# Optimization experiments

Measured on AMD Instinct MI355X. Metric: run time of the kernel, lower is better.

The kernel has to match this reference:

```python
import jax, jax.numpy as jnp
import numpy as np

# ---- config constants (from configs) ----
B, L, C = 32, 512, 16
DM, DS, DCONV, EXP, EL = 128, 16, 4, 2, 2
PATCH, STRIDE, PAD, PRED = 16, 8, 8, 96
DIN = EXP * DM            # 256
DTR = (DM + 15) // 16     # dt_rank = 8
NPATCH = (L + 2 * PAD - PATCH) // STRIDE + 1   # 65
HNF = DM * NPATCH         # 8320
EPS = 1e-5


def setup_inputs() -> dict:
    key = jax.random.key(0)
    ks = jax.random.split(key, 14)
    n = jax.random.normal
    A_log = jnp.tile(jnp.log(jnp.arange(1, DS + 1, dtype=jnp.float32)), (EL, DIN, 1))
    return {
        "x_enc": n(ks[0], (B, L, C), jnp.float32),
        "x_mark_enc": n(ks[1], (B, L, 4), jnp.float32),
        "pe_w": n(ks[2], (DM, 1, PATCH), jnp.float32) * (1.0 / np.sqrt(PATCH)),
        "pe_b": n(ks[3], (DM,), jnp.float32) * 0.02,
        "in_proj_w": n(ks[4], (EL, 2 * DIN, DM), jnp.float32) * (1.0 / np.sqrt(DM)),
        "conv_w": n(ks[5], (EL, DIN, DCONV), jnp.float32) * (1.0 / np.sqrt(DCONV)),
        "conv_b": n(ks[6], (EL, DIN), jnp.float32) * 0.02,
        "x_proj_w": n(ks[7], (EL, DTR + 2 * DS, DIN), jnp.float32) * (1.0 / np.sqrt(DIN)),
        "dt_proj_w": n(ks[8], (EL, DIN, DTR), jnp.float32) * (1.0 / np.sqrt(DTR)),
        "dt_proj_b": n(ks[9], (EL, DIN), jnp.float32) * 0.1,
        "A_log": A_log,
        "D": jnp.ones((EL, DIN), jnp.float32),
        "out_proj_w": n(ks[10], (EL, DM, DIN), jnp.float32) * (1.0 / np.sqrt(DIN)),
        "head_w": n(ks[11], (PRED, HNF), jnp.float32) * (1.0 / np.sqrt(HNF)),
    }


def _silu(x):
    return x * jax.nn.sigmoid(x)


def _mamba(x, in_w, cw, cb, xp_w, dtp_w, dtp_b, A_log, Dp, out_w):
    # x: (b, P, DM)
    b = x.shape[0]
    xz = jnp.einsum('bpd,ed->bpe', x, in_w)            # (b, P, 2*DIN)
    xin, z = jnp.split(xz, 2, axis=-1)
    # causal depthwise conv1d over time
    xt = xin.transpose(0, 2, 1)                        # (b, DIN, P)
    conv = jax.lax.conv_general_dilated(
        xt, cw[:, None, :], (1,), [(DCONV - 1, 0)],
        dimension_numbers=('NCH', 'OIH', 'NCH'), feature_group_count=DIN)
    xc = _silu((conv + cb[None, :, None]).transpose(0, 2, 1))   # (b, P, DIN)
    dbc = jnp.einsum('bpd,ed->bpe', xc, xp_w)          # (b, P, DTR+2*DS)
    dt, Bm, Cm = jnp.split(dbc, [DTR, DTR + DS], axis=-1)
    dt = jax.nn.softplus(jnp.einsum('bpr,dr->bpd', dt, dtp_w) + dtp_b)  # (b,P,DIN)
    A = -jnp.exp(A_log)                                # (DIN, DS)

    def step(h, inp):
        dt_t, B_t, C_t, x_t = inp                      # (b,DIN),(b,DS),(b,DS),(b,DIN)
        dA = jnp.exp(dt_t[:, :, None] * A)             # (b,DIN,DS)
        h = dA * h + (dt_t * x_t)[:, :, None] * B_t[:, None, :]
        y = jnp.einsum('bds,bs->bd', h, C_t)
        return h, y

    h0 = jnp.zeros((b, DIN, DS), x.dtype)
    xs = (dt.transpose(1, 0, 2), Bm.transpose(1, 0, 2),
          Cm.transpose(1, 0, 2), xc.transpose(1, 0, 2))
    _, ys = jax.lax.scan(step, h0, xs)                 # (P, b, DIN)
    y = ys.transpose(1, 0, 2) + xc * Dp
    y = y * _silu(z)
    return jnp.einsum('bpd,od->bpo', y, out_w)         # (b, P, DM)


def reference(x_enc, x_mark_enc, pe_w, pe_b, in_proj_w, conv_w, conv_b,
              x_proj_w, dt_proj_w, dt_proj_b, A_log, D, out_proj_w, head_w):
    # RevIN-style normalization (stats detached, as in torch)
    mean = jax.lax.stop_gradient(jnp.mean(x_enc, axis=1, keepdims=True))
    xc = x_enc - mean
    std = jax.lax.stop_gradient(jnp.sqrt(jnp.var(xc, axis=1, keepdims=True) + EPS))
    xn = xc / std                                      # (B, L, C)
    x = xn.transpose(0, 2, 1).reshape(B * C, 1, L)
    # patch embedding conv
    p = jax.lax.conv_general_dilated(
        x, pe_w, (STRIDE,), [(PAD, PAD)],
        dimension_numbers=('NCH', 'OIH', 'NCH')) + pe_b[None, :, None]
    p = p.transpose(0, 2, 1)                           # (B*C, NPATCH, DM)
    for i in range(EL):
        p = _mamba(p, in_proj_w[i], conv_w[i], conv_b[i], x_proj_w[i],
                   dt_proj_w[i], dt_proj_b[i], A_log[i], D[i], out_proj_w[i])
    flat = p.reshape(B * C, HNF)
    head = flat @ head_w.T                             # (B*C, PRED)
    out = head.reshape(B, C, PRED).transpose(0, 2, 1)  # (B, PRED, C)
    return out * std + mean
```

## Files before the change

### kernel.cpp

```cpp
#include <hip/hip_runtime.h>

typedef __attribute__((ext_vector_type(8))) short bf16x8;
typedef __attribute__((ext_vector_type(8))) unsigned short u16x8;
typedef __attribute__((ext_vector_type(4))) float f32x4;

#define DEV static __device__ __forceinline__

constexpr int DM   = 128;
constexpr int DIN  = 256;
constexpr int NP   = 65;
constexpr int NSEQ = 512;
constexpr int HNF  = 8320;
constexpr int LOPL = NSEQ*HNF;

constexpr size_t OFF_FLAG = 0;
constexpr size_t OFF_MEAN = 16;
constexpr size_t OFF_STD  = OFF_MEAN + 512;
constexpr size_t OFF_ANEG = OFF_STD  + 512;
constexpr size_t OFF_CONVW= OFF_ANEG + 8192;
constexpr size_t OFF_CONVB= OFF_CONVW+ 2048;
constexpr size_t OFF_DTPB = OFF_CONVB+ 512;
constexpr size_t OFF_DD   = OFF_DTPB + 512;
constexpr size_t OFF_PEWT = OFF_DD   + 512;
constexpr size_t OFF_PEB  = OFF_PEWT + 2048;
constexpr size_t OFF_INF  = OFF_PEB  + 128;
constexpr size_t OFF_XPF  = OFF_INF  + 65536;
constexpr size_t OFF_OPF  = OFF_XPF  + 12288;
constexpr size_t OFF_HDF  = OFF_OPF  + 32768;
constexpr size_t OFF_PA   = OFF_HDF  + 399360;
constexpr size_t OFF_PB   = OFF_PA   + (size_t)NSEQ*HNF;
constexpr size_t OFF_HACC = OFF_PB;

DEV float b2f(unsigned short u){ union{unsigned v; float f;} x; x.v = ((unsigned)u)<<16; return x.f; }
DEV unsigned short f2b(float f){
  union{float f32; unsigned u;} x; x.f32 = f;
  unsigned r = x.u + 0x7fffu + ((x.u>>16)&1u);
  return (unsigned short)(r>>16);
}
DEV void split2(float v, unsigned short& h, unsigned short& l){
  h = f2b(v); l = f2b(v - b2f(h));
}
DEV float load_in(const void* p, size_t i, int isbf){
  return isbf ? b2f(((const unsigned short*)p)[i]) : ((const float*)p)[i];
}
DEV f32x4 mfma16(bf16x8 a, bf16x8 b, f32x4 c){
  return __builtin_amdgcn_mfma_f32_16x16x32_bf16(a,b,c,0,0,0);
}
constexpr float LOG2E = 1.4426950408889634f;
constexpr float LN2   = 0.6931471805599453f;
DEV float ex2(float x){ float r; asm("v_exp_f32 %0, %1" : "=v"(r) : "v"(x)); return r; }
DEV float lg2(float x){ float r; asm("v_log_f32 %0, %1" : "=v"(r) : "v"(x)); return r; }
DEV float frcp(float x){ float r; asm("v_rcp_f32 %0, %1" : "=v"(r) : "v"(x)); return r; }
DEV float sigm(float x){ return frcp(1.f + ex2(-x*LOG2E)); }
DEV float softplus(float x){
  float t = ex2(-fabsf(x)*LOG2E);
  return fmaxf(x,0.f) + LN2*lg2(1.f + t);
}
DEV int detect_bf16_wave(const void* x, int tid){
  const unsigned short* u = (const unsigned short*)x;
  unsigned short v = u[2*tid];
  int e = (v>>7)&0xff;
  int pred = (v==0) || (e>=100 && e<=141);
  unsigned long long m = __ballot(pred);
  return __popcll(m) >= 48;
}
DEV u16x8 load8_cvt(const void* p, size_t off, int isbf){
  u16x8 o;
  if (isbf){
    o = *(const u16x8*)((const unsigned short*)p + off);
  } else {
    const float* s = (const float*)p + off;
    float4 a = *(const float4*)(s), b = *(const float4*)(s+4);
    o[0]=f2b(a.x); o[1]=f2b(a.y); o[2]=f2b(a.z); o[3]=f2b(a.w);
    o[4]=f2b(b.x); o[5]=f2b(b.y); o[6]=f2b(b.z); o[7]=f2b(b.w);
  }
  return o;
}

constexpr size_t N_SMALL = 13952;
constexpr size_t N_IN8 = 16384, N_XP8 = 3072, N_OP8 = 8192, N_HD8 = 99840;
constexpr size_t N_BIG8 = N_IN8+N_XP8+N_OP8+N_HD8;
constexpr int NPREP = (int)((N_SMALL + N_BIG8 + 255)/256);
__global__ void k_pre(const void* x_enc, const void* pe_w, const void* pe_b,
                      const void* in_w, const void* conv_w, const void* conv_b,
                      const void* xp_w, const void* dtp_b,
                      const void* A_log, const void* Dm, const void* op_w,
                      const void* head_w, float* __restrict__ ws)
{
  const int tid = threadIdx.x;
  __shared__ int sflag;
  __shared__ float sx[512];
  __shared__ float spe[16*128];
  __shared__ float spb[128];
  __shared__ float rs[8], rq[8], sm[2];

  if (tid < 64){
    int f = detect_bf16_wave(x_enc, tid);
    if (tid==0) sflag = f;
  }
  __syncthreads();
  const int isbf = sflag;

  if (blockIdx.x < NPREP){
    if (blockIdx.x==0 && tid==0) ws[OFF_FLAG] = (float)isbf;
    size_t i = (size_t)blockIdx.x*256 + tid;
    const size_t nA=8192, nCW=2048, nCB=512, nDB=512, nD=512, nPW=2048, nPB=128;
    if (i < N_SMALL){
      if (i < nA){ ws[OFF_ANEG+i] = -__expf(load_in(A_log,i,isbf)); return; } i -= nA;
      if (i < nCW){ ws[OFF_CONVW+i] = load_in(conv_w,i,isbf); return; } i -= nCW;
      if (i < nCB){ ws[OFF_CONVB+i] = load_in(conv_b,i,isbf); return; } i -= nCB;
      if (i < nDB){ ws[OFF_DTPB+i]  = load_in(dtp_b,i,isbf); return; } i -= nDB;
      if (i < nD){  ws[OFF_DD+i]    = load_in(Dm,i,isbf); return; } i -= nD;
      if (i < nPW){ size_t k=i>>7, dm=i&127; ws[OFF_PEWT+i]=load_in(pe_w, dm*16+k, isbf); return; } i -= nPW;
      ws[OFF_PEB+i] = load_in(pe_b,i,isbf); return;
    }
    size_t i8 = i - N_SMALL;
    if (i8 >= N_BIG8) return;
    if (i8 < N_IN8){
      size_t lane=i8&63, kk=(i8>>6)&3, nt=(i8>>8)&31, l=i8>>13;
      size_t e=nt*16+(lane&15), k0=kk*32+((lane>>4)*8);
      ((u16x8*)((unsigned short*)(ws+OFF_INF)))[i8] =
        load8_cvt(in_w, (l*512+e)*128 + k0, isbf);
      return;
    } i8 -= N_IN8;
    if (i8 < N_XP8){
      size_t lane=i8&63, kk=(i8>>6)&7; size_t rest=i8>>9;
      size_t nt=rest%3, l=rest/3;
      size_t o=nt*16+(lane&15), k0=kk*32+((lane>>4)*8);
      u16x8 v;
      if (o<40) v = load8_cvt(xp_w, (l*40+o)*256 + k0, isbf);
      else { u16x8 z = {0,0,0,0,0,0,0,0}; v = z; }
      ((u16x8*)((unsigned short*)(ws+OFF_XPF)))[i8] = v;
      return;
    } i8 -= N_XP8;
    if (i8 < N_OP8){
      size_t lane=i8&63, kk=(i8>>6)&7, nt=(i8>>9)&7, l=i8>>12;
      size_t dm=nt*16+(lane&15), k0=kk*32+((lane>>4)*8);
      ((u16x8*)((unsigned short*)(ws+OFF_OPF)))[i8] =
        load8_cvt(op_w, (l*128+dm)*256 + k0, isbf);
      return;
    } i8 -= N_OP8;
    {
      size_t lane=i8&63, t=i8>>6;
      size_t kk=t%260, nt=t/260;
      size_t pr=nt*16+(lane&15), k0=kk*32+((lane>>4)*8);
      ((u16x8*)((unsigned short*)(ws+OFF_HDF)))[i8] =
        load8_cvt(head_w, pr*8320 + k0, isbf);
      return;
    }
  }

  const int n = blockIdx.x - NPREP;
  const int b = n>>4, c = n&15;

  float v0 = load_in(x_enc, ((size_t)b*512+tid)*16 + c, isbf);
  float v1 = load_in(x_enc, ((size_t)b*512+tid+256)*16 + c, isbf);
  float s = v0+v1, q = v0*v0+v1*v1;
  for (int o=32;o;o>>=1){ s += __shfl_down(s,o,64); q += __shfl_down(q,o,64); }
  const int w = tid>>6, lane = tid&63;
  if (lane==0){ rs[w]=s; rq[w]=q; }
  __syncthreads();
  if (tid==0){
    float S=rs[0]+rs[1]+rs[2]+rs[3], Q=rq[0]+rq[1]+rq[2]+rq[3];
    float mean = S*(1.f/512.f);
    float var = fmaxf(Q*(1.f/512.f)-mean*mean, 0.f);
    float sd = sqrtf(var+1e-5f);
    sm[0]=mean; sm[1]=1.f/sd;
    ws[OFF_MEAN+n]=mean; ws[OFF_STD+n]=sd;
  }
  __syncthreads();
  const float mean=sm[0], rstd=sm[1];
  sx[tid]=(v0-mean)*rstd; sx[tid+256]=(v1-mean)*rstd;
  for (int i=tid;i<2048;i+=256) spe[i]=load_in(pe_w, (size_t)(i&127)*16 + (i>>7), isbf);
  if (tid<128) spb[tid]=load_in(pe_b, tid, isbf);
  __syncthreads();

  unsigned short* pa_hi = (unsigned short*)(ws+OFF_PA);
  unsigned short* pa_lo = pa_hi + LOPL;
  for (int i=tid;i<NP*DM;i+=256){
    int t=i>>7, dm=i&127;
    float acc = spb[dm];
    int j0 = t*8-8;
    #pragma unroll
    for (int k=0;k<16;k++){ int j=j0+k; if ((unsigned)j<512u) acc += sx[j]*spe[k*128+dm]; }
    unsigned short h,lo2; split2(acc,h,lo2);
    pa_hi[(size_t)n*HNF+i] = h;
    pa_lo[(size_t)n*HNF+i] = lo2;
  }
}

__global__ __launch_bounds__(256,2)
void k_layer(int l, const unsigned short* __restrict__ pin,
             unsigned short* __restrict__ pout, float* __restrict__ ws,
             const void* __restrict__ dtp_w_raw)
{
  const int n = blockIdx.x, tid = threadIdx.x;
  const int w = tid>>6, lane = tid&63, ml = lane&15, quad = lane>>4;
  const int isbf = ws[OFF_FLAG] != 0.f;

  __shared__ __align__(16) unsigned char arena[79040];
  unsigned short* s_hi = (unsigned short*)arena;
  unsigned short* s_lo = (unsigned short*)(arena+34320);
  float* s_dbc = (float*)(arena+68640);

  const unsigned short* INF = (const unsigned short*)(ws+OFF_INF) + (size_t)l*65536;
  const unsigned short* XPF = (const unsigned short*)(ws+OFF_XPF) + (size_t)l*12288;
  const unsigned short* OPF = (const unsigned short*)(ws+OFF_OPF) + (size_t)l*32768;
  const unsigned short* phi = pin + (size_t)n*HNF;
  const unsigned short* plo = phi + LOPL;

  for (int pass=0; pass<2; ++pass){
    f32x4 acc[5][2];
    #pragma unroll
    for (int mt=0;mt<5;mt++){
      #pragma unroll
      for (int p2=0;p2<2;p2++){ f32x4 z={0.f,0.f,0.f,0.f}; acc[mt][p2]=z; }
    }
    bf16x8 ah[2][5], al[2][5];
    #pragma unroll
    for (int mt=0;mt<5;mt++){
      int row = mt*16+ml; if (row>64) row=64;
      ah[0][mt] = *(const bf16x8*)&phi[(size_t)row*128 + quad*8];
      al[0][mt] = *(const bf16x8*)&plo[(size_t)row*128 + quad*8];
    }
    #pragma unroll
    for (int kk=0;kk<4;kk++){
      const int cur = kk&1, nxt = cur^1;
      bf16x8 b0 = *(const bf16x8*)&INF[((size_t)((pass*8+w*2+0)*4+kk))*512 + lane*8];
      bf16x8 b1 = *(const bf16x8*)&INF[((size_t)((pass*8+w*2+1)*4+kk))*512 + lane*8];
      if (kk<3){
        #pragma unroll
        for (int mt=0;mt<5;mt++){
          int row = mt*16+ml; if (row>64) row=64;
          ah[nxt][mt] = *(const bf16x8*)&phi[(size_t)row*128 + (kk+1)*32 + quad*8];
          al[nxt][mt] = *(const bf16x8*)&plo[(size_t)row*128 + (kk+1)*32 + quad*8];
        }
      }
      #pragma unroll
      for (int mt=0;mt<5;mt++)
        acc[mt][0] = mfma16(ah[cur][mt],b0,mfma16(al[cur][mt],b0,acc[mt][0]));
      #pragma unroll
      for (int mt=0;mt<5;mt++)
        acc[mt][1] = mfma16(ah[cur][mt],b1,mfma16(al[cur][mt],b1,acc[mt][1]));
    }
    #pragma unroll
    for (int p2=0;p2<2;p2++){
      int e = (pass*8 + w*2 + p2)*16 + ml;
      #pragma unroll
      for (int mt=0;mt<5;mt++){
        #pragma unroll
        for (int r=0;r<4;r++){
          int t = mt*16+quad*4+r;
          if (t<NP){
            unsigned short h,lo2; split2(acc[mt][p2][r],h,lo2);
            s_hi[t*264+e]=h; s_lo[t*264+e]=lo2;
          }
        }
      }
    }
  }
  __syncthreads();

  {
    const int d = tid;
    const float4 wv = ((const float4*)(ws+OFF_CONVW))[l*256+d];
    const float bb = ws[OFF_CONVB + l*256+d];
    float x0=0.f,x1=0.f,x2=0.f;
    int t = 0;
    for (; t+4<=NP; t+=4){
      float xi0 = b2f(s_hi[(t+0)*264+d]) + b2f(s_lo[(t+0)*264+d]);
      float xi1 = b2f(s_hi[(t+1)*264+d]) + b2f(s_lo[(t+1)*264+d]);
      float xi2 = b2f(s_hi[(t+2)*264+d]) + b2f(s_lo[(t+2)*264+d]);
      float xi3 = b2f(s_hi[(t+3)*264+d]) + b2f(s_lo[(t+3)*264+d]);
      float v0 = bb + wv.x*x0  + wv.y*x1  + wv.z*x2  + wv.w*xi0;
      float v1 = bb + wv.x*x1  + wv.y*x2  + wv.z*xi0 + wv.w*xi1;
      float v2 = bb + wv.x*x2  + wv.y*xi0 + wv.z*xi1 + wv.w*xi2;
      float v3 = bb + wv.x*xi0 + wv.y*xi1 + wv.z*xi2 + wv.w*xi3;
      x0=xi1; x1=xi2; x2=xi3;
      float s0 = v0*sigm(v0), s1 = v1*sigm(v1), s2 = v2*sigm(v2), s3 = v3*sigm(v3);
      unsigned short h,lo2;
      split2(s0,h,lo2); s_hi[(t+0)*264+d]=h; s_lo[(t+0)*264+d]=lo2;
      split2(s1,h,lo2); s_hi[(t+1)*264+d]=h; s_lo[(t+1)*264+d]=lo2;
      split2(s2,h,lo2); s_hi[(t+2)*264+d]=h; s_lo[(t+2)*264+d]=lo2;
      split2(s3,h,lo2); s_hi[(t+3)*264+d]=h; s_lo[(t+3)*264+d]=lo2;
    }
    for (; t<NP; ++t){
      float xi = b2f(s_hi[t*264+d]) + b2f(s_lo[t*264+d]);
      float v = bb + wv.x*x0 + wv.y*x1 + wv.z*x2 + wv.w*xi;
      x0=x1; x1=x2; x2=xi;
      float sv = v * sigm(v);
      unsigned short h,lo2; split2(sv,h,lo2);
      s_hi[t*264+d]=h; s_lo[t*264+d]=lo2;
    }
  }
  __syncthreads();

  for (int tile=w; tile<15; tile+=4){
    int mt=tile/3, nt=tile%3;
    f32x4 acc={0.f,0.f,0.f,0.f};
    #pragma unroll
    for (int kk=0;kk<8;kk++){
      int row = mt*16+ml; if (row>64) row=64;
      bf16x8 ah = *(const bf16x8*)&s_hi[row*264 + kk*32 + quad*8];
      bf16x8 al = *(const bf16x8*)&s_lo[row*264 + kk*32 + quad*8];
      bf16x8 b  = *(const bf16x8*)&XPF[((size_t)(nt*8+kk))*512 + lane*8];
      acc = mfma16(ah,b,mfma16(al,b,acc));
    }
    int o = nt*16+ml;
    #pragma unroll
    for (int r=0;r<4;r++){
      int t=mt*16+quad*4+r;
      if (t<NP && o<40) s_dbc[t*40+o] = acc[r];
    }
  }
  __syncthreads();

  {
    const int d = tid;
    float A2[16];
    {
      const float4* ap = (const float4*)(ws+OFF_ANEG) + ((size_t)l*256+d)*4;
      #pragma unroll
      for (int qq=0;qq<4;qq++){
        float4 t4 = ap[qq];
        A2[qq*4]=t4.x*LOG2E; A2[qq*4+1]=t4.y*LOG2E; A2[qq*4+2]=t4.z*LOG2E; A2[qq*4+3]=t4.w*LOG2E;
      }
    }
    int fastbit = 1;
    #pragma unroll
    for (int ss=0;ss<16;ss++){
      float ex = -(float)(ss+1)*LOG2E;
      fastbit &= (fabsf(A2[ss]-ex) <= 1e-4f*(float)(ss+1)) ? 1 : 0;
    }
    const int fastu = __all(fastbit);
    const float Dv = ws[OFF_DD + l*256+d];
    const float bias = ws[OFF_DTPB + l*256+d];
    float wdt[8];
    #pragma unroll
    for (int r=0;r<8;r++) wdt[r] = load_in(dtp_w_raw, ((size_t)l*256+d)*8+r, isbf);
    float h[16];
    #pragma unroll
    for (int ss=0;ss<16;ss++) h[ss]=0.f;

    float4 q0 = *(const float4*)&s_dbc[0];
    float4 q1 = *(const float4*)&s_dbc[4];
    float xh = b2f(s_hi[d]), xl = b2f(s_lo[d]);

    for (int t=0;t<NP;t++){
      const float* row = &s_dbc[t*40];
      float xv = xh + xl;
      float4 b0=*(const float4*)(row+8),  b1=*(const float4*)(row+12),
             b2v=*(const float4*)(row+16), b3=*(const float4*)(row+20);
      float4 c0=*(const float4*)(row+24), c1=*(const float4*)(row+28),
             c2=*(const float4*)(row+32), c3=*(const float4*)(row+36);
      float4 nq0, nq1; float nxh=0.f, nxl=0.f;
      if (t+1<NP){
        const float* nrow = &s_dbc[(t+1)*40];
        nq0 = *(const float4*)(nrow);
        nq1 = *(const float4*)(nrow+4);
        nxh = b2f(s_hi[(t+1)*264+d]); nxl = b2f(s_lo[(t+1)*264+d]);
      }
      float p0 = q0.x*wdt[0] + q0.y*wdt[1];
      float p1 = q0.z*wdt[2] + q0.w*wdt[3];
      float p2 = q1.x*wdt[4] + q1.y*wdt[5];
      float p3 = q1.z*wdt[6] + q1.w*wdt[7];
      float din = (bias + p0 + p1) + (p2 + p3);
      float dtv = softplus(din);
      float dtx = dtv*xv;
      float Bv[16], Cv[16];
      Bv[0]=b0.x;Bv[1]=b0.y;Bv[2]=b0.z;Bv[3]=b0.w; Bv[4]=b1.x;Bv[5]=b1.y;Bv[6]=b1.z;Bv[7]=b1.w;
      Bv[8]=b2v.x;Bv[9]=b2v.y;Bv[10]=b2v.z;Bv[11]=b2v.w; Bv[12]=b3.x;Bv[13]=b3.y;Bv[14]=b3.z;Bv[15]=b3.w;
      Cv[0]=c0.x;Cv[1]=c0.y;Cv[2]=c0.z;Cv[3]=c0.w; Cv[4]=c1.x;Cv[5]=c1.y;Cv[6]=c1.z;Cv[7]=c1.w;
      Cv[8]=c2.x;Cv[9]=c2.y;Cv[10]=c2.z;Cv[11]=c2.w; Cv[12]=c3.x;Cv[13]=c3.y;Cv[14]=c3.z;Cv[15]=c3.w;
      float rr[16];
      if (fastu){
        float r1 = ex2(-dtv*LOG2E);
        float r2=r1*r1;
        float r3=r2*r1, r4=r2*r2;
        float r5=r4*r1, r6=r4*r2, r7=r4*r3, r8=r4*r4;
        rr[0]=r1; rr[1]=r2; rr[2]=r3; rr[3]=r4;
        rr[4]=r5; rr[5]=r6; rr[6]=r7; rr[7]=r8;
        rr[8]=r8*r1; rr[9]=r8*r2; rr[10]=r8*r3; rr[11]=r8*r4;
        rr[12]=r8*r5; rr[13]=r8*r6; rr[14]=r8*r7; rr[15]=r8*r8;
      } else {
        #pragma unroll
        for (int ss=0;ss<16;ss++) rr[ss] = ex2(dtv*A2[ss]);
      }
      float y0 = 0.f, y1 = 0.f;
      #pragma unroll
      for (int ss=0;ss<16;ss+=2){
        h[ss]   = rr[ss]*h[ss]     + dtx*Bv[ss];
        h[ss+1] = rr[ss+1]*h[ss+1] + dtx*Bv[ss+1];
        y0 += h[ss]*Cv[ss];
        y1 += h[ss+1]*Cv[ss+1];
      }
      float g0 = (y0+y1) + xv*Dv;
      unsigned short hh,lo2; split2(g0,hh,lo2);
      s_hi[t*264+d]=hh; s_lo[t*264+d]=lo2;
      q0=nq0; q1=nq1; xh=nxh; xl=nxl;
    }
  }
  __syncthreads();

  {
    bf16x8 ah[2][4], al[2][4];
    {
      int row = ml;
      #pragma unroll
      for (int kk=0;kk<4;kk++){
        ah[0][kk] = *(const bf16x8*)&phi[(size_t)row*128 + kk*32 + quad*8];
        al[0][kk] = *(const bf16x8*)&plo[(size_t)row*128 + kk*32 + quad*8];
      }
    }
    #pragma unroll
    for (int mt=0; mt<5; ++mt){
      const int cur = mt&1, nxt = cur^1;
      if (mt<4){
        int row = (mt+1)*16+ml; if (row>64) row=64;
        #pragma unroll
        for (int kk=0;kk<4;kk++){
          ah[nxt][kk] = *(const bf16x8*)&phi[(size_t)row*128 + kk*32 + quad*8];
          al[nxt][kk] = *(const bf16x8*)&plo[(size_t)row*128 + kk*32 + quad*8];
        }
      }
      #pragma unroll
      for (int j=0;j<4;j++){
        int nt = w + j*4;
        f32x4 acc={0.f,0.f,0.f,0.f};
        #pragma unroll
        for (int kk=0;kk<4;kk++){
          bf16x8 b = *(const bf16x8*)&INF[((size_t)((16+nt)*4+kk))*512 + lane*8];
          acc = mfma16(ah[cur][kk],b,mfma16(al[cur][kk],b,acc));
        }
        int d = nt*16+ml;
        #pragma unroll
        for (int r=0;r<4;r++){
          int t = mt*16+quad*4+r;
          if (t<NP){
            float g0 = b2f(s_hi[t*264+d]) + b2f(s_lo[t*264+d]);
            float zv = acc[r];
            float g = g0 * zv * sigm(zv);
            unsigned short hh,lo2; split2(g,hh,lo2);
            s_hi[t*264+d]=hh; s_lo[t*264+d]=lo2;
          }
        }
      }
    }
  }
  __syncthreads();

  {
    f32x4 acc[5][2];
    #pragma unroll
    for (int mt=0;mt<5;mt++){
      #pragma unroll
      for (int p2=0;p2<2;p2++){ f32x4 z={0.f,0.f,0.f,0.f}; acc[mt][p2]=z; }
    }
    bf16x8 bpre[2][2];
    bpre[0][0] = *(const bf16x8*)&OPF[((size_t)((w*2+0)*8+0))*512 + lane*8];
    bpre[0][1] = *(const bf16x8*)&OPF[((size_t)((w*2+1)*8+0))*512 + lane*8];
    #pragma unroll
    for (int kk=0;kk<8;kk++){
      const int cur = kk&1, nxt = cur^1;
      if (kk<7){
        bpre[nxt][0] = *(const bf16x8*)&OPF[((size_t)((w*2+0)*8+kk+1))*512 + lane*8];
        bpre[nxt][1] = *(const bf16x8*)&OPF[((size_t)((w*2+1)*8+kk+1))*512 + lane*8];
      }
      bf16x8 ah[5], al[5];
      #pragma unroll
      for (int mt=0;mt<5;mt++){
        int row = mt*16+ml; if (row>64) row=64;
        ah[mt] = *(const bf16x8*)&s_hi[row*264 + kk*32 + quad*8];
        al[mt] = *(const bf16x8*)&s_lo[row*264 + kk*32 + quad*8];
      }
      #pragma unroll
      for (int mt=0;mt<5;mt++)
        acc[mt][0] = mfma16(ah[mt],bpre[cur][0],mfma16(al[mt],bpre[cur][0],acc[mt][0]));
      #pragma unroll
      for (int mt=0;mt<5;mt++)
        acc[mt][1] = mfma16(ah[mt],bpre[cur][1],mfma16(al[mt],bpre[cur][1],acc[mt][1]));
    }
    #pragma unroll
    for (int p2=0;p2<2;p2++){
      int dm = (w*2+p2)*16+ml;
      #pragma unroll
      for (int mt=0;mt<5;mt++){
        #pragma unroll
        for (int r=0;r<4;r++){
          int t = mt*16+quad*4+r;
          if (t<NP){
            unsigned short hh,lo2; split2(acc[mt][p2][r],hh,lo2);
            pout[(size_t)n*HNF + t*128 + dm] = hh;
            pout[(size_t)n*HNF + t*128 + dm + LOPL] = lo2;
          }
        }
      }
    }
  }
}

__global__ void k_headp(const float* __restrict__ ws, float* __restrict__ hacc)
{
  const int blk = blockIdx.x;
  const int p = blk & 3, tile = blk >> 2;
  const int nt = tile%6, mt = tile/6;
  const int tid = threadIdx.x, w = tid>>6, lane = tid&63, ml = lane&15, quad = lane>>4;
  const unsigned short* pa_hi = (const unsigned short*)(ws+OFF_PA);
  const unsigned short* pa_lo = pa_hi + LOPL;
  const unsigned short* HDF = (const unsigned short*)(ws+OFF_HDF);
  __shared__ float red[4][64][4];

  f32x4 acc={0.f,0.f,0.f,0.f};
  const size_t abase = (size_t)(mt*16+ml)*HNF + quad*8;
  int i = w;
  int kk = p*65 + i;
  bf16x8 ah = *(const bf16x8*)(pa_hi + abase + (size_t)kk*32);
  bf16x8 al = *(const bf16x8*)(pa_lo + abase + (size_t)kk*32);
  bf16x8 b  = *(const bf16x8*)&HDF[((size_t)(nt*260+kk))*512 + lane*8];
  while (i < 65){
    const int inext = i + 4;
    bf16x8 nah, nal, nb;
    if (inext < 65){
      int nkk = p*65 + inext;
      nah = *(const bf16x8*)(pa_hi + abase + (size_t)nkk*32);
      nal = *(const bf16x8*)(pa_lo + abase + (size_t)nkk*32);
      nb  = *(const bf16x8*)&HDF[((size_t)(nt*260+nkk))*512 + lane*8];
    }
    acc = mfma16(ah,b,mfma16(al,b,acc));
    ah=nah; al=nal; b=nb; i=inext;
  }
  #pragma unroll
  for (int r=0;r<4;r++) red[w][lane][r]=acc[r];
  __syncthreads();
  if (w==0){
    #pragma unroll
    for (int r=0;r<4;r++){
      float s = red[0][lane][r]+red[1][lane][r]+red[2][lane][r]+red[3][lane][r];
      hacc[((size_t)tile*4 + p)*256 + lane*4 + r] = s;
    }
  }
}

__global__ void k_fin(const float* __restrict__ ws, void* __restrict__ out)
{
  const int tile = blockIdx.x;
  const int nt = tile%6, mt = tile/6;
  const int lane = threadIdx.x, ml = lane&15, quad = lane>>4;
  const float* hacc = ws + OFF_HACC;
  const int isbf = ws[OFF_FLAG]!=0.f;
  #pragma unroll
  for (int r=0;r<4;r++){
    size_t base = (size_t)tile*4*256 + lane*4 + r;
    float s = hacc[base] + hacc[base+256] + hacc[base+512] + hacc[base+768];
    int nseq = mt*16 + quad*4 + r;
    int pred = nt*16 + ml;
    float val = s*ws[OFF_STD+nseq] + ws[OFF_MEAN+nseq];
    size_t o = ((size_t)(nseq>>4)*96 + pred)*16 + (nseq&15);
    if (isbf) ((unsigned short*)out)[o] = f2b(val);
    else      ((float*)out)[o] = val;
  }
}

extern "C" void kernel_launch(void* const* d_in, const int* in_sizes, int n_in,
                              void* d_out, int out_size, void* d_ws, size_t ws_size,
                              hipStream_t stream)
{
  (void)in_sizes; (void)n_in; (void)out_size; (void)ws_size;
  float* ws = (float*)d_ws;
  const void* x_enc = d_in[0];
  const void* pe_w  = d_in[2];  const void* pe_b  = d_in[3];
  const void* in_w  = d_in[4];  const void* conv_w= d_in[5];
  const void* conv_b= d_in[6];  const void* xp_w  = d_in[7];
  const void* dtp_w = d_in[8];  const void* dtp_b = d_in[9];
  const void* A_log = d_in[10]; const void* Dm    = d_in[11];
  const void* op_w  = d_in[12]; const void* head_w= d_in[13];

  k_pre<<<NPREP+NSEQ,256,0,stream>>>(x_enc,pe_w,pe_b,in_w,conv_w,conv_b,xp_w,
                                     dtp_b,A_log,Dm,op_w,head_w,ws);
  unsigned short* pa = (unsigned short*)(ws+OFF_PA);
  unsigned short* pb = (unsigned short*)(ws+OFF_PB);
  k_layer<<<NSEQ,256,0,stream>>>(0,pa,pb,ws,dtp_w);
  k_layer<<<NSEQ,256,0,stream>>>(1,pb,pa,ws,dtp_w);
  k_headp<<<768,256,0,stream>>>(ws, ws+OFF_HACC);
  k_fin<<<192,64,0,stream>>>(ws, d_out);
}
```

Baseline: 264.4 us.

## Double k_layer block to 512 threads and split scan states across thread pairs

Launches the per-sequence Mamba layer kernel with 512 threads instead of 256. The in_proj passes are spread over 8 waves, and the conv is split into two time halves with boundary state preloaded. The selective scan splits the 16 SSM states across two lanes that combine their outputs with a shuffle. Out_proj uses one N-tile per wave. This targets the serial per-thread scan latency and low parallelism per block, at the cost of more threads per block, lower per-CU occupancy given the large LDS arena, and extra syncs and shuffles.

```diff
diff --git a/kernel.cpp b/kernel.cpp
--- a/kernel.cpp
+++ b/kernel.cpp
@@ -189,7 +189,7 @@
   }
 }
 
-__global__ __launch_bounds__(256,2)
+__global__ __launch_bounds__(512,2)
 void k_layer(int l, const unsigned short* __restrict__ pin,
              unsigned short* __restrict__ pout, float* __restrict__ ws,
              const void* __restrict__ dtp_w_raw)
@@ -202,6 +202,7 @@
   unsigned short* s_hi = (unsigned short*)arena;
   unsigned short* s_lo = (unsigned short*)(arena+34320);
   float* s_dbc = (float*)(arena+68640);
+  constexpr int LOH = 17160;
 
   const unsigned short* INF = (const unsigned short*)(ws+OFF_INF) + (size_t)l*65536;
   const unsigned short* XPF = (const unsigned short*)(ws+OFF_XPF) + (size_t)l*12288;
@@ -209,7 +210,7 @@
   const unsigned short* phi = pin + (size_t)n*HNF;
   const unsigned short* plo = phi + LOPL;
 
-  for (int pass=0; pass<2; ++pass){
+  {
     f32x4 acc[5][2];
     #pragma unroll
     for (int mt=0;mt<5;mt++){
@@ -226,8 +227,8 @@
     #pragma unroll
     for (int kk=0;kk<4;kk++){
       const int cur = kk&1, nxt = cur^1;
-      bf16x8 b0 = *(const bf16x8*)&INF[((size_t)((pass*8+w*2+0)*4+kk))*512 + lane*8];
-      bf16x8 b1 = *(const bf16x8*)&INF[((size_t)((pass*8+w*2+1)*4+kk))*512 + lane*8];
+      bf16x8 b0 = *(const bf16x8*)&INF[((size_t)((w*2+0)*4+kk))*512 + lane*8];
+      bf16x8 b1 = *(const bf16x8*)&INF[((size_t)((w*2+1)*4+kk))*512 + lane*8];
       if (kk<3){
         #pragma unroll
         for (int mt=0;mt<5;mt++){
@@ -245,7 +246,7 @@
     }
     #pragma unroll
     for (int p2=0;p2<2;p2++){
-      int e = (pass*8 + w*2 + p2)*16 + ml;
+      int e = (w*2 + p2)*16 + ml;
       #pragma unroll
       for (int mt=0;mt<5;mt++){
         #pragma unroll
@@ -262,12 +263,19 @@
   __syncthreads();
 
   {
-    const int d = tid;
+    const int d = tid & 255, half = tid >> 8;
     const float4 wv = ((const float4*)(ws+OFF_CONVW))[l*256+d];
     const float bb = ws[OFF_CONVB + l*256+d];
-    float x0=0.f,x1=0.f,x2=0.f;
-    int t = 0;
-    for (; t+4<=NP; t+=4){
+    float x0=0.f, x1=0.f, x2=0.f;
+    if (half){
+      x0 = b2f(s_hi[30*264+d]) + b2f(s_lo[30*264+d]);
+      x1 = b2f(s_hi[31*264+d]) + b2f(s_lo[31*264+d]);
+      x2 = b2f(s_hi[32*264+d]) + b2f(s_lo[32*264+d]);
+    }
+    __syncthreads();
+    const int t0 = half ? 33 : 0, t1 = half ? NP : 33;
+    int t = t0;
+    for (; t+4<=t1; t+=4){
       float xi0 = b2f(s_hi[(t+0)*264+d]) + b2f(s_lo[(t+0)*264+d]);
       float xi1 = b2f(s_hi[(t+1)*264+d]) + b2f(s_lo[(t+1)*264+d]);
       float xi2 = b2f(s_hi[(t+2)*264+d]) + b2f(s_lo[(t+2)*264+d]);
@@ -284,7 +292,7 @@
       split2(s2,h,lo2); s_hi[(t+2)*264+d]=h; s_lo[(t+2)*264+d]=lo2;
       split2(s3,h,lo2); s_hi[(t+3)*264+d]=h; s_lo[(t+3)*264+d]=lo2;
     }
-    for (; t<NP; ++t){
+    for (; t<t1; ++t){
       float xi = b2f(s_hi[t*264+d]) + b2f(s_lo[t*264+d]);
       float v = bb + wv.x*x0 + wv.y*x1 + wv.z*x2 + wv.w*xi;
       x0=x1; x1=x2; x2=xi;
@@ -295,7 +303,7 @@
   }
   __syncthreads();
 
-  for (int tile=w; tile<15; tile+=4){
+  for (int tile=w; tile<15; tile+=8){
     int mt=tile/3, nt=tile%3;
     f32x4 acc={0.f,0.f,0.f,0.f};
     #pragma unroll
@@ -316,21 +324,21 @@
   __syncthreads();
 
   {
-    const int d = tid;
-    float A2[16];
+    const int d = (tid>>1) & 255;
+    const int ho = tid & 1;
+    float A2[8];
     {
-      const float4* ap = (const float4*)(ws+OFF_ANEG) + ((size_t)l*256+d)*4;
-      #pragma unroll
-      for (int qq=0;qq<4;qq++){
-        float4 t4 = ap[qq];
-        A2[qq*4]=t4.x*LOG2E; A2[qq*4+1]=t4.y*LOG2E; A2[qq*4+2]=t4.z*LOG2E; A2[qq*4+3]=t4.w*LOG2E;
-      }
+      const float4* ap = (const float4*)(ws+OFF_ANEG) + ((size_t)l*256+d)*4 + ho*2;
+      float4 ta = ap[0], tb = ap[1];
+      A2[0]=ta.x*LOG2E; A2[1]=ta.y*LOG2E; A2[2]=ta.z*LOG2E; A2[3]=ta.w*LOG2E;
+      A2[4]=tb.x*LOG2E; A2[5]=tb.y*LOG2E; A2[6]=tb.z*LOG2E; A2[7]=tb.w*LOG2E;
     }
     int fastbit = 1;
     #pragma unroll
-    for (int ss=0;ss<16;ss++){
-      float ex = -(float)(ss+1)*LOG2E;
-      fastbit &= (fabsf(A2[ss]-ex) <= 1e-4f*(float)(ss+1)) ? 1 : 0;
+    for (int ss=0;ss<8;ss++){
+      int sidx = ho*8 + ss + 1;
+      float ex = -(float)sidx*LOG2E;
+      fastbit &= (fabsf(A2[ss]-ex) <= 1e-4f*(float)sidx) ? 1 : 0;
     }
     const int fastu = __all(fastbit);
     const float Dv = ws[OFF_DD + l*256+d];
@@ -338,9 +346,9 @@
     float wdt[8];
     #pragma unroll
     for (int r=0;r<8;r++) wdt[r] = load_in(dtp_w_raw, ((size_t)l*256+d)*8+r, isbf);
-    float h[16];
-    #pragma unroll
-    for (int ss=0;ss<16;ss++) h[ss]=0.f;
+    float h[8];
+    #pragma unroll
+    for (int ss=0;ss<8;ss++) h[ss]=0.f;
 
     float4 q0 = *(const float4*)&s_dbc[0];
     float4 q1 = *(const float4*)&s_dbc[4];
@@ -349,10 +357,10 @@
     for (int t=0;t<NP;t++){
       const float* row = &s_dbc[t*40];
       float xv = xh + xl;
-      float4 b0=*(const float4*)(row+8),  b1=*(const float4*)(row+12),
-             b2v=*(const float4*)(row+16), b3=*(const float4*)(row+20);
-      float4 c0=*(const float4*)(row+24), c1=*(const float4*)(row+28),
-             c2=*(const float4*)(row+32), c3=*(const float4*)(row+36);
+      const float* bp = row + 8 + ho*8;
+      const float* cp = row + 24 + ho*8;
+      float4 b0=*(const float4*)(bp), b1=*(const float4*)(bp+4);
+      float4 c0=*(const float4*)(cp), c1=*(const float4*)(cp+4);
       float4 nq0, nq1; float nxh=0.f, nxl=0.f;
       if (t+1<NP){
         const float* nrow = &s_dbc[(t+1)*40];
@@ -367,36 +375,35 @@
       float din = (bias + p0 + p1) + (p2 + p3);
       float dtv = softplus(din);
       float dtx = dtv*xv;
-      float Bv[16], Cv[16];
+      float Bv[8], Cv[8];
       Bv[0]=b0.x;Bv[1]=b0.y;Bv[2]=b0.z;Bv[3]=b0.w; Bv[4]=b1.x;Bv[5]=b1.y;Bv[6]=b1.z;Bv[7]=b1.w;
-      Bv[8]=b2v.x;Bv[9]=b2v.y;Bv[10]=b2v.z;Bv[11]=b2v.w; Bv[12]=b3.x;Bv[13]=b3.y;Bv[14]=b3.z;Bv[15]=b3.w;
       Cv[0]=c0.x;Cv[1]=c0.y;Cv[2]=c0.z;Cv[3]=c0.w; Cv[4]=c1.x;Cv[5]=c1.y;Cv[6]=c1.z;Cv[7]=c1.w;
-      Cv[8]=c2.x;Cv[9]=c2.y;Cv[10]=c2.z;Cv[11]=c2.w; Cv[12]=c3.x;Cv[13]=c3.y;Cv[14]=c3.z;Cv[15]=c3.w;
-      float rr[16];
+      float rr[8];
       if (fastu){
         float r1 = ex2(-dtv*LOG2E);
-        float r2=r1*r1;
-        float r3=r2*r1, r4=r2*r2;
+        float r2=r1*r1, r3=r2*r1, r4=r2*r2;
         float r5=r4*r1, r6=r4*r2, r7=r4*r3, r8=r4*r4;
-        rr[0]=r1; rr[1]=r2; rr[2]=r3; rr[3]=r4;
-        rr[4]=r5; rr[5]=r6; rr[6]=r7; rr[7]=r8;
-        rr[8]=r8*r1; rr[9]=r8*r2; rr[10]=r8*r3; rr[11]=r8*r4;
-        rr[12]=r8*r5; rr[13]=r8*r6; rr[14]=r8*r7; rr[15]=r8*r8;
+        float rp = ho ? r8 : 1.f;
+        rr[0]=r1*rp; rr[1]=r2*rp; rr[2]=r3*rp; rr[3]=r4*rp;
+        rr[4]=r5*rp; rr[5]=r6*rp; rr[6]=r7*rp; rr[7]=r8*rp;
       } else {
         #pragma unroll
-        for (int ss=0;ss<16;ss++) rr[ss] = ex2(dtv*A2[ss]);
+        for (int ss=0;ss<8;ss++) rr[ss] = ex2(dtv*A2[ss]);
       }
       float y0 = 0.f, y1 = 0.f;
       #pragma unroll
-      for (int ss=0;ss<16;ss+=2){
+      for (int ss=0;ss<8;ss+=2){
         h[ss]   = rr[ss]*h[ss]     + dtx*Bv[ss];
         h[ss+1] = rr[ss+1]*h[ss+1] + dtx*Bv[ss+1];
         y0 += h[ss]*Cv[ss];
         y1 += h[ss+1]*Cv[ss+1];
       }
-      float g0 = (y0+y1) + xv*Dv;
+      float y = y0 + y1;
+      y += __shfl_xor(y, 1, 64);
+      float g0 = y + xv*Dv;
       unsigned short hh,lo2; split2(g0,hh,lo2);
-      s_hi[t*264+d]=hh; s_lo[t*264+d]=lo2;
+      unsigned short vv = ho ? lo2 : hh;
+      s_hi[t*264 + d + ho*LOH] = vv;
       q0=nq0; q1=nq1; xh=nxh; xl=nxl;
     }
   }
@@ -424,8 +431,8 @@
         }
       }
       #pragma unroll
-      for (int j=0;j<4;j++){
-        int nt = w + j*4;
+      for (int j=0;j<2;j++){
+        int nt = w + j*8;
         f32x4 acc={0.f,0.f,0.f,0.f};
         #pragma unroll
         for (int kk=0;kk<4;kk++){
@@ -450,22 +457,16 @@
   __syncthreads();
 
   {
-    f32x4 acc[5][2];
-    #pragma unroll
-    for (int mt=0;mt<5;mt++){
-      #pragma unroll
-      for (int p2=0;p2<2;p2++){ f32x4 z={0.f,0.f,0.f,0.f}; acc[mt][p2]=z; }
-    }
-    bf16x8 bpre[2][2];
-    bpre[0][0] = *(const bf16x8*)&OPF[((size_t)((w*2+0)*8+0))*512 + lane*8];
-    bpre[0][1] = *(const bf16x8*)&OPF[((size_t)((w*2+1)*8+0))*512 + lane*8];
+    f32x4 acc[5];
+    #pragma unroll
+    for (int mt=0;mt<5;mt++){ f32x4 z={0.f,0.f,0.f,0.f}; acc[mt]=z; }
+    bf16x8 bpre[2];
+    bpre[0] = *(const bf16x8*)&OPF[((size_t)(w*8+0))*512 + lane*8];
     #pragma unroll
     for (int kk=0;kk<8;kk++){
       const int cur = kk&1, nxt = cur^1;
-      if (kk<7){
-        bpre[nxt][0] = *(const bf16x8*)&OPF[((size_t)((w*2+0)*8+kk+1))*512 + lane*8];
-        bpre[nxt][1] = *(const bf16x8*)&OPF[((size_t)((w*2+1)*8+kk+1))*512 + lane*8];
-      }
+      if (kk<7)
+        bpre[nxt] = *(const bf16x8*)&OPF[((size_t)(w*8+kk+1))*512 + lane*8];
       bf16x8 ah[5], al[5];
       #pragma unroll
       for (int mt=0;mt<5;mt++){
@@ -475,24 +476,18 @@
       }
       #pragma unroll
       for (int mt=0;mt<5;mt++)
-        acc[mt][0] = mfma16(ah[mt],bpre[cur][0],mfma16(al[mt],bpre[cur][0],acc[mt][0]));
-      #pragma unroll
-      for (int mt=0;mt<5;mt++)
-        acc[mt][1] = mfma16(ah[mt],bpre[cur][1],mfma16(al[mt],bpre[cur][1],acc[mt][1]));
-    }
-    #pragma unroll
-    for (int p2=0;p2<2;p2++){
-      int dm = (w*2+p2)*16+ml;
-      #pragma unroll
-      for (int mt=0;mt<5;mt++){
-        #pragma unroll
-        for (int r=0;r<4;r++){
-          int t = mt*16+quad*4+r;
-          if (t<NP){
-            unsigned short hh,lo2; split2(acc[mt][p2][r],hh,lo2);
-            pout[(size_t)n*HNF + t*128 + dm] = hh;
-            pout[(size_t)n*HNF + t*128 + dm + LOPL] = lo2;
-          }
+        acc[mt] = mfma16(ah[mt],bpre[cur],mfma16(al[mt],bpre[cur],acc[mt]));
+    }
+    int dm = w*16+ml;
+    #pragma unroll
+    for (int mt=0;mt<5;mt++){
+      #pragma unroll
+      for (int r=0;r<4;r++){
+        int t = mt*16+quad*4+r;
+        if (t<NP){
+          unsigned short hh,lo2; split2(acc[mt][r],hh,lo2);
+          pout[(size_t)n*HNF + t*128 + dm] = hh;
+          pout[(size_t)n*HNF + t*128 + dm + LOPL] = lo2;
         }
       }
     }
@@ -579,8 +574,8 @@
                                      dtp_b,A_log,Dm,op_w,head_w,ws);
   unsigned short* pa = (unsigned short*)(ws+OFF_PA);
   unsigned short* pb = (unsigned short*)(ws+OFF_PB);
-  k_layer<<<NSEQ,256,0,stream>>>(0,pa,pb,ws,dtp_w);
-  k_layer<<<NSEQ,256,0,stream>>>(1,pb,pa,ws,dtp_w);
+  k_layer<<<NSEQ,512,0,stream>>>(0,pa,pb,ws,dtp_w);
+  k_layer<<<NSEQ,512,0,stream>>>(1,pb,pa,ws,dtp_w);
   k_headp<<<768,256,0,stream>>>(ws, ws+OFF_HACC);
   k_fin<<<192,64,0,stream>>>(ws, d_out);
 }
```

Result: slower. 322.9 us (+22.1%).
